# Kernel tuning notes

Measured on AMD Instinct MI355X. Metric: run time of the kernel, lower is better.

## Reference

```python
import jax, jax.numpy as jnp
import numpy as np

N0, N1, N2 = 400000, 75000, 15000
E1, E2 = 1200000, 240000
F_IN, NC = 64, 40
H1, C1 = 2, 8          # layer 1: heads=2, out_channels=8 -> concat dim 16
H2, C2 = 1, NC         # layer 2: heads=1, out_channels=num_classes
NEG_SLOPE = 0.2


def gat_conv(x_src, x_dst, src, dst, Ws, Wd, att_s, att_d, bias, heads, ch):
    """PyG GATConv on bipartite (x_src, x_dst) with remove+add self loops."""
    n_dst = x_dst.shape[0]
    hs = (x_src @ Ws).reshape(-1, heads, ch)   # [N_src, H, C]
    hd = (x_dst @ Wd).reshape(-1, heads, ch)   # [N_dst, H, C]
    a_s = (hs * att_s).sum(-1)                 # [N_src, H]
    a_d = (hd * att_d).sum(-1)                 # [N_dst, H]
    loops = jnp.arange(n_dst)
    src_all = jnp.concatenate([src, loops])
    dst_all = jnp.concatenate([dst, loops])
    # remove_self_loops: drop pre-existing i->i edges; add_self_loops: appended
    valid = jnp.concatenate([src != dst, jnp.ones(n_dst, dtype=bool)])[:, None]
    logits = jax.nn.leaky_relu(a_s[src_all] + a_d[dst_all], NEG_SLOPE)  # [E, H]
    logits = jnp.where(valid, logits, -jnp.inf)
    m = jax.ops.segment_max(logits, dst_all, num_segments=n_dst)        # [N_dst, H]
    w = jnp.where(valid, jnp.exp(logits - m[dst_all]), 0.0)
    denom = jax.ops.segment_sum(w, dst_all, num_segments=n_dst)
    alpha = w / denom[dst_all]                                          # [E, H]
    out = jax.ops.segment_sum(alpha[:, :, None] * hs[src_all], dst_all,
                              num_segments=n_dst)                       # [N_dst, H, C]
    return out.reshape(n_dst, heads * ch) + bias


def setup_inputs() -> dict:
    key = jax.random.key(0)
    ks = jax.random.split(key, 16)
    s = 0.1
    return {
        "x": jax.random.normal(ks[0], (N0, F_IN), dtype=jnp.float32),
        "e1_src": jax.random.randint(ks[1], (E1,), 0, N0),
        "e1_dst": jax.random.randint(ks[2], (E1,), 0, N1),
        "e2_src": jax.random.randint(ks[3], (E2,), 0, N1),
        "e2_dst": jax.random.randint(ks[4], (E2,), 0, N2),
        "W1s": jax.random.normal(ks[5], (F_IN, H1 * C1), dtype=jnp.float32) * s,
        "W1d": jax.random.normal(ks[6], (F_IN, H1 * C1), dtype=jnp.float32) * s,
        "att1_s": jax.random.normal(ks[7], (H1, C1), dtype=jnp.float32) * s,
        "att1_d": jax.random.normal(ks[8], (H1, C1), dtype=jnp.float32) * s,
        "b1": jnp.zeros((H1 * C1,), dtype=jnp.float32),
        "W2s": jax.random.normal(ks[9], (H1 * C1, H2 * C2), dtype=jnp.float32) * s,
        "W2d": jax.random.normal(ks[10], (H1 * C1, H2 * C2), dtype=jnp.float32) * s,
        "att2_s": jax.random.normal(ks[11], (H2, C2), dtype=jnp.float32) * s,
        "att2_d": jax.random.normal(ks[12], (H2, C2), dtype=jnp.float32) * s,
        "b2": jnp.zeros((H2 * C2,), dtype=jnp.float32),
    }


def reference(x, e1_src, e1_dst, e2_src, e2_dst,
              W1s, W1d, att1_s, att1_d, b1,
              W2s, W2d, att2_s, att2_d, b2):
    h = gat_conv(x, x[:N1], e1_src, e1_dst, W1s, W1d, att1_s, att1_d, b1, H1, C1)
    h = jax.nn.elu(h)
    o = gat_conv(h, h[:N2], e2_src, e2_dst, W2s, W2d, att2_s, att2_d, b2, H2, C2)
    return jax.nn.log_softmax(o, axis=-1)
```

## Files before the change

### kernel.cpp

```cpp
#include <hip/hip_runtime.h>
#include <hip/hip_bf16.h>

constexpr int N0 = 400000, N1 = 75000, N2 = 15000;
constexpr int E1 = 1200000, E2 = 240000;
constexpr int NC = 40;
constexpr float NEG_SLOPE = 0.2f;

constexpr int BK1 = 128;
constexpr int NB1 = (N1 + BK1 - 1) / BK1;
constexpr int CAPB1 = 2432;
constexpr int BK2 = 32;
constexpr int NB2 = (N2 + BK2 - 1) / BK2;
constexpr int CAPB2 = 704;

constexpr int TILE = 8192;
constexpr int NT1 = (E1 + TILE - 1) / TILE;
constexpr int NT2 = (E2 + TILE - 1) / TILE;
constexpr int BPJ = (N0 + 511) / 512;

using f32x4 = __attribute__((ext_vector_type(4))) float;
using s16x8 = __attribute__((ext_vector_type(8))) short;

__device__ __forceinline__ float leaky(float v) { return v > 0.f ? v : NEG_SLOPE * v; }

__device__ __forceinline__ unsigned cvtpk(float lo, float hi) {
    unsigned r;
    asm("v_cvt_pk_bf16_f32 %0, %1, %2" : "=v"(r) : "v"(lo), "v"(hi));
    return r;
}

__device__ __forceinline__ unsigned bf16pair(float lo, float hi) {
    unsigned a = __float_as_uint(lo), b = __float_as_uint(hi);
    a = (a + 0x7FFFu + ((a >> 16) & 1u)) >> 16;
    b = (b + 0x7FFFu + ((b >> 16) & 1u)) & 0xFFFF0000u;
    return a | b;
}
__device__ __forceinline__ float bfLo(unsigned w) { return __uint_as_float(w << 16); }
__device__ __forceinline__ float bfHi(unsigned w) { return __uint_as_float(w & 0xFFFF0000u); }

__global__ __launch_bounds__(256) void k1a_kernel(
    const int* __restrict__ e1s, const int* __restrict__ e1d,
    const int* __restrict__ e2s, const int* __restrict__ e2d,
    int* __restrict__ gcnt1, unsigned* __restrict__ bin1,
    int* __restrict__ gcnt2, unsigned* __restrict__ bin2)
{
    __shared__ int hist[NB1];
    __shared__ int gbase[NB1];

    const int bid = blockIdx.x;
    const int tid = threadIdx.x;
    const bool isL1 = bid < NT1;
    const int* es = isL1 ? e1s : e2s;
    const int* ed = isL1 ? e1d : e2d;
    const int nE = isL1 ? E1 : E2;
    const int nb = isL1 ? NB1 : NB2;
    const int cap = isL1 ? CAPB1 : CAPB2;
    const int shift = isL1 ? 7 : 5;
    const int lsh = isL1 ? 19 : 17;
    int* gc = isL1 ? gcnt1 : gcnt2;
    unsigned* gbin = isL1 ? bin1 : bin2;
    const int base = (isL1 ? bid : bid - NT1) * TILE;
    const int lim = min(TILE, nE - base);

    for (int b = tid; b < nb; b += 256) hist[b] = 0;
    __syncthreads();
    for (int i = tid; i < lim; i += 256) {
        int s = es[base + i], d = ed[base + i];
        if (s != d) atomicAdd(&hist[d >> shift], 1);
    }
    __syncthreads();
    for (int b = tid; b < nb; b += 256) {
        int c = hist[b];
        gbase[b] = (c > 0) ? atomicAdd(&gc[b], c) : 0;
        hist[b] = 0;
    }
    __syncthreads();
    for (int i = tid; i < lim; i += 256) {
        int s = es[base + i], d = ed[base + i];
        if (s != d) {
            int b = d >> shift;
            int pos = gbase[b] + atomicAdd(&hist[b], 1);
            if (pos < cap)
                gbin[(size_t)b * cap + pos] =
                    (unsigned)s | ((unsigned)(d & ((1 << shift) - 1)) << lsh);
        }
    }
}

__global__ __launch_bounds__(256, 2) void k1b_kernel(
    const float* __restrict__ x,
    const float* __restrict__ W1s, const float* __restrict__ W1d,
    const float* __restrict__ att1s, const float* __restrict__ att1d,
    unsigned* __restrict__ rec1, float* __restrict__ a_d1)
{
    __shared__ float2 vds[64];
    const int tid = threadIdx.x;
    const int l = tid & 63, nd = l & 15, kg = l >> 4, wv = tid >> 6;
    const int nodeBase = blockIdx.x * 512;
    const bool hasN1 = nodeBase < N1;

    if (hasN1) {
        if (tid < 64) {
            float d0 = 0.f, d1 = 0.f;
            const float* wr = W1d + (size_t)tid * 16;
            #pragma unroll
            for (int cc = 0; cc < 8; ++cc) {
                d0 = fmaf(wr[cc], att1d[cc], d0);
                d1 = fmaf(wr[8 + cc], att1d[8 + cc], d1);
            }
            vds[tid] = make_float2(d0, d1);
        }
        __syncthreads();
    }

    s16x8 bf0, bf1;
    {
        union { unsigned u[4]; s16x8 v; } t0, t1;
        #pragma unroll
        for (int q = 0; q < 4; ++q) {
            t0.u[q] = cvtpk(W1s[(8 * kg + 2 * q) * 16 + nd],
                            W1s[(8 * kg + 2 * q + 1) * 16 + nd]);
            t1.u[q] = cvtpk(W1s[(32 + 8 * kg + 2 * q) * 16 + nd],
                            W1s[(32 + 8 * kg + 2 * q + 1) * 16 + nd]);
        }
        bf0 = t0.v; bf1 = t1.v;
    }
    float att4[4];
    #pragma unroll
    for (int r = 0; r < 4; ++r) att4[r] = att1s[4 * kg + r];

    const int myBase = nodeBase + wv * 16 + nd;

    float4 P[4][4];

    auto LOADr = [&](int r, float4 (&Q)[4]) {
        int n = min(myBase + r * 64, N0 - 1);
        const float* xr_ = x + (size_t)n * 64 + 8 * kg;
        Q[0] = *(const float4*)(xr_);
        Q[1] = *(const float4*)(xr_ + 4);
        Q[2] = *(const float4*)(xr_ + 32);
        Q[3] = *(const float4*)(xr_ + 36);
    };

    #pragma unroll
    for (int r = 0; r < 4; ++r) LOADr(r, P[r]);

    #pragma unroll
    for (int r = 0; r < 8; ++r) {
        const int node = myBase + r * 64;
        float4 (&Q)[4] = P[r & 3];

        union { unsigned u[4]; s16x8 v; } a0, a1;
        a0.u[0] = cvtpk(Q[0].x, Q[0].y); a0.u[1] = cvtpk(Q[0].z, Q[0].w);
        a0.u[2] = cvtpk(Q[1].x, Q[1].y); a0.u[3] = cvtpk(Q[1].z, Q[1].w);
        a1.u[0] = cvtpk(Q[2].x, Q[2].y); a1.u[1] = cvtpk(Q[2].z, Q[2].w);
        a1.u[2] = cvtpk(Q[3].x, Q[3].y); a1.u[3] = cvtpk(Q[3].z, Q[3].w);

        float pd0 = 0.f, pd1 = 0.f;
        if (hasN1) {
            float xv8[16] = {Q[0].x, Q[0].y, Q[0].z, Q[0].w, Q[1].x, Q[1].y, Q[1].z, Q[1].w,
                             Q[2].x, Q[2].y, Q[2].z, Q[2].w, Q[3].x, Q[3].y, Q[3].z, Q[3].w};
            #pragma unroll
            for (int j = 0; j < 8; ++j) {
                float2 v = vds[8 * kg + j];
                pd0 = fmaf(xv8[j], v.x, pd0);
                pd1 = fmaf(xv8[j], v.y, pd1);
            }
            #pragma unroll
            for (int j = 0; j < 8; ++j) {
                float2 v = vds[32 + 8 * kg + j];
                pd0 = fmaf(xv8[8 + j], v.x, pd0);
                pd1 = fmaf(xv8[8 + j], v.y, pd1);
            }
        }

        if (r + 4 < 8) LOADr(r + 4, Q);
        __builtin_amdgcn_sched_barrier(0);

        f32x4 acc = {0.f, 0.f, 0.f, 0.f};
        acc = __builtin_amdgcn_mfma_f32_16x16x32_bf16(bf0, a0.v, acc, 0, 0, 0);
        acc = __builtin_amdgcn_mfma_f32_16x16x32_bf16(bf1, a1.v, acc, 0, 0, 0);

        float p = acc[0] * att4[0];
        p = fmaf(acc[1], att4[1], p);
        p = fmaf(acc[2], att4[2], p);
        p = fmaf(acc[3], att4[3], p);
        p += __shfl_xor(p, 16, 64);
        float q = __shfl_xor(p, 32, 64);

        if (node < N0) {
            unsigned* rp = rec1 + (size_t)node * 16;
            uint2 hw;
            hw.x = cvtpk(acc[0], acc[1]);
            hw.y = cvtpk(acc[2], acc[3]);
            *(uint2*)(rp + 2 * kg) = hw;
            if (kg == 0)
                *(uint4*)(rp + 8) = make_uint4(__float_as_uint(p), __float_as_uint(q), 0u, 0u);
            else if (kg == 1)
                *(uint4*)(rp + 12) = make_uint4(0u, 0u, 0u, 0u);
        }
        if (hasN1 && node < N1) {
            pd0 += __shfl_xor(pd0, 16, 64); pd0 += __shfl_xor(pd0, 32, 64);
            pd1 += __shfl_xor(pd1, 16, 64); pd1 += __shfl_xor(pd1, 32, 64);
            if (kg == 0)
                ((float2*)a_d1)[node] = make_float2(pd0, pd1);
        }
    }
}

__global__ __launch_bounds__(512) void k2_kernel(
    const int* __restrict__ gcnt1, const unsigned* __restrict__ bin1,
    const unsigned* __restrict__ rec1, const float* __restrict__ a_d1,
    const float* __restrict__ b1,
    const float* __restrict__ W2s, const float* __restrict__ W2d,
    const float* __restrict__ att2s, const float* __restrict__ att2d,
    unsigned* __restrict__ rec2)
{
    __shared__ unsigned srt[CAPB1];
    __shared__ int hist[BK1], start[BK1 + 1];
    __shared__ float w2sl[640], va[16], vd[16];
    __shared__ float h1s[BK1][17];

    const int b = blockIdx.x, tid = threadIdx.x;
    const int d0 = b * BK1;
    const int nN = min(BK1, N1 - d0);
    const int ncnt = min(gcnt1[b], CAPB1);
    const unsigned* bp = bin1 + (size_t)b * CAPB1;

    for (int i = tid; i < 640; i += 512) w2sl[i] = W2s[i];
    if (tid < BK1) hist[tid] = 0;
    if (tid >= 128 && tid < 144) {
        int k = tid - 128;
        float sa = 0.f, sd = 0.f;
        for (int cc = 0; cc < 40; ++cc) {
            sa = fmaf(W2s[k * 40 + cc], att2s[cc], sa);
            sd = fmaf(W2d[k * 40 + cc], att2d[cc], sd);
        }
        va[k] = sa; vd[k] = sd;
    }
    __syncthreads();
    for (int i = tid; i < ncnt; i += 512) atomicAdd(&hist[bp[i] >> 19], 1);
    __syncthreads();
    if (tid == 0) {
        int a = 0;
        for (int k = 0; k < BK1; ++k) { start[k] = a; a += hist[k]; }
        start[BK1] = a;
    }
    __syncthreads();
    if (tid < BK1) hist[tid] = start[tid];
    __syncthreads();
    for (int i = tid; i < ncnt; i += 512) {
        unsigned p = bp[i];
        int pos = atomicAdd(&hist[p >> 19], 1);
        srt[pos] = p & 0x7FFFFu;
    }
    __syncthreads();

    const int g = tid >> 4, c = tid & 15, h = c >> 3;
    const int wbase = tid & 48;
    const int wmap = (c < 8) ? c : (8 + ((c >> 2) & 1));
    for (int n = g; n < nN; n += 32) {
        const int node = d0 + n;
        const float ad = a_d1[(size_t)node * 2 + h];
        const int st = start[n], cnt = start[n + 1] - start[n];
        unsigned rw0 = rec1[(size_t)node * 16 + wmap];
        unsigned rw1 = (cnt >= 1) ? rec1[(size_t)srt[st] * 16 + wmap] : 0u;
        unsigned rw2 = (cnt >= 2) ? rec1[(size_t)srt[st + 1] * 16 + wmap] : 0u;
        unsigned rw3 = (cnt >= 3) ? rec1[(size_t)srt[st + 2] * 16 + wmap] : 0u;
        float accv = 0.f, den = 0.f;
        for (int j = 0; j <= cnt; ++j) {
            float asv = __uint_as_float((unsigned)__shfl((int)rw0, wbase + 8 + 4 * h, 64));
            unsigned chw = (unsigned)__shfl((int)rw0, wbase + (c >> 1), 64);
            float hv = (c & 1) ? bfHi(chw) : bfLo(chw);
            float w = __expf(leaky(asv + ad));
            accv = fmaf(w, hv, accv);
            den += w;
            rw0 = rw1; rw1 = rw2; rw2 = rw3;
            rw3 = (j + 4 <= cnt) ? rec1[(size_t)srt[st + j + 3] * 16 + wmap] : 0u;
        }
        float v = accv / den + b1[c];
        h1s[n][c] = v > 0.f ? v : (__expf(v) - 1.f);
    }
    __syncthreads();
    for (int i = tid; i < nN * 24; i += 512) {
        int nn = i / 24, w = i - nn * 24;
        unsigned* rp = rec2 + (size_t)(d0 + nn) * 24;
        if (w < 20) {
            int c0 = 2 * w, c1 = c0 + 1;
            float s0 = 0.f, s1 = 0.f;
            #pragma unroll
            for (int k = 0; k < 16; ++k) {
                float hk = h1s[nn][k];
                s0 = fmaf(hk, w2sl[k * 40 + c0], s0);
                s1 = fmaf(hk, w2sl[k * 40 + c1], s1);
            }
            rp[w] = bf16pair(s0, s1);
        } else if (w < 22) {
            const float* vv = (w == 20) ? va : vd;
            float s = 0.f;
            #pragma unroll
            for (int k = 0; k < 16; ++k) s = fmaf(h1s[nn][k], vv[k], s);
            rp[w] = __float_as_uint(s);
        }
    }
}

__global__ __launch_bounds__(1024) void k3_kernel(
    const int* __restrict__ gcnt2, const unsigned* __restrict__ bin2,
    const unsigned* __restrict__ rec2, const float* __restrict__ b2,
    float* __restrict__ out)
{
    __shared__ unsigned srt[CAPB2];
    __shared__ int hist[BK2], start[BK2 + 1];

    const int b = blockIdx.x, tid = threadIdx.x;
    const int d0 = b * BK2;
    const int nN = min(BK2, N2 - d0);
    const int ncnt = min(gcnt2[b], CAPB2);
    const unsigned* bp = bin2 + (size_t)b * CAPB2;

    if (tid < BK2) hist[tid] = 0;
    __syncthreads();
    for (int i = tid; i < ncnt; i += 1024) atomicAdd(&hist[bp[i] >> 17], 1);
    __syncthreads();
    if (tid == 0) {
        int a = 0;
        for (int k = 0; k < BK2; ++k) { start[k] = a; a += hist[k]; }
        start[BK2] = a;
    }
    __syncthreads();
    if (tid < BK2) hist[tid] = start[tid];
    __syncthreads();
    for (int i = tid; i < ncnt; i += 1024) {
        unsigned p = bp[i];
        int pos = atomicAdd(&hist[p >> 17], 1);
        srt[pos] = p & 0x1FFFFu;
    }
    __syncthreads();

    const int g = tid >> 5, l = tid & 31;
    const float bb0 = (l < 20) ? b2[2 * l] : 0.f;
    const float bb1 = (l < 20) ? b2[2 * l + 1] : 0.f;
    for (int n = g; n < nN; n += 32) {
        const int node = d0 + n;
        const int st = start[n], cnt = start[n + 1] - start[n];
        unsigned rw0 = (l < 22) ? rec2[(size_t)node * 24 + l] : 0u;
        const float ad = __uint_as_float((unsigned)__shfl((int)rw0, 21, 32));
        unsigned rw1 = (cnt >= 1 && l < 21) ? rec2[(size_t)srt[st] * 24 + l] : 0u;
        unsigned rw2 = (cnt >= 2 && l < 21) ? rec2[(size_t)srt[st + 1] * 24 + l] : 0u;
        unsigned rw3 = (cnt >= 3 && l < 21) ? rec2[(size_t)srt[st + 2] * 24 + l] : 0u;
        float a0 = 0.f, a1 = 0.f, den = 0.f;
        for (int j = 0; j <= cnt; ++j) {
            float asv = __uint_as_float((unsigned)__shfl((int)rw0, 20, 32));
            float w = __expf(leaky(asv + ad));
            a0 = fmaf(w, bfLo(rw0), a0);
            a1 = fmaf(w, bfHi(rw0), a1);
            den += w;
            rw0 = rw1; rw1 = rw2; rw2 = rw3;
            rw3 = (j + 4 <= cnt && l < 21) ? rec2[(size_t)srt[st + j + 3] * 24 + l] : 0u;
        }
        float v0 = (l < 20) ? a0 / den + bb0 : -3.4e38f;
        float v1 = (l < 20) ? a1 / den + bb1 : -3.4e38f;
        float mx = fmaxf(v0, v1);
        #pragma unroll
        for (int k = 16; k >= 1; k >>= 1) mx = fmaxf(mx, __shfl_xor(mx, k, 32));
        float ex = (l < 20) ? __expf(v0 - mx) + __expf(v1 - mx) : 0.f;
        #pragma unroll
        for (int k = 16; k >= 1; k >>= 1) ex += __shfl_xor(ex, k, 32);
        float lse = mx + logf(ex);
        if (l < 20)
            ((float2*)(out + (size_t)node * 40))[l] = make_float2(v0 - lse, v1 - lse);
    }
}

extern "C" void kernel_launch(void* const* d_in, const int* in_sizes, int n_in,
                              void* d_out, int out_size, void* d_ws, size_t ws_size,
                              hipStream_t stream) {
    const float* x      = (const float*)d_in[0];
    const int*   e1_src = (const int*)d_in[1];
    const int*   e1_dst = (const int*)d_in[2];
    const int*   e2_src = (const int*)d_in[3];
    const int*   e2_dst = (const int*)d_in[4];
    const float* W1s    = (const float*)d_in[5];
    const float* W1d    = (const float*)d_in[6];
    const float* att1s  = (const float*)d_in[7];
    const float* att1d  = (const float*)d_in[8];
    const float* b1     = (const float*)d_in[9];
    const float* W2s    = (const float*)d_in[10];
    const float* W2d    = (const float*)d_in[11];
    const float* att2s  = (const float*)d_in[12];
    const float* att2d  = (const float*)d_in[13];
    const float* b2     = (const float*)d_in[14];
    float* out = (float*)d_out;

    float* wsbase = (float*)d_ws;
    size_t o = 0;
    int*      gcnt1 = (int*)(wsbase + o);      o += NB1;
    int*      gcnt2 = (int*)(wsbase + o);      o += NB2;
    const size_t zeroWords = o;
    unsigned* bin1  = (unsigned*)(wsbase + o); o += (size_t)NB1 * CAPB1;
    unsigned* bin2  = (unsigned*)(wsbase + o); o += (size_t)NB2 * CAPB2;
    unsigned* rec1  = (unsigned*)(wsbase + o); o += (size_t)N0 * 16;
    float*    a_d1  = (float*)(wsbase + o);    o += (size_t)N1 * 2;
    unsigned* rec2  = (unsigned*)(wsbase + o); o += (size_t)N1 * 24;

    hipMemsetAsync(d_ws, 0, zeroWords * sizeof(float), stream);

    k1a_kernel<<<NT1 + NT2, 256, 0, stream>>>(
        e1_src, e1_dst, e2_src, e2_dst, gcnt1, bin1, gcnt2, bin2);

    k1b_kernel<<<BPJ, 256, 0, stream>>>(
        x, W1s, W1d, att1s, att1d, rec1, a_d1);

    k2_kernel<<<NB1, 512, 0, stream>>>(gcnt1, bin1, rec1, a_d1, b1,
                                       W2s, W2d, att2s, att2d, rec2);

    k3_kernel<<<NB2, 1024, 0, stream>>>(gcnt2, bin2, rec2, b2, out);
}
```

Measured before the change: 133.9 us.

## Fuse edge binning and layer-1 projection into one kernel launch with one node tile per block

Merges the edge-binning kernel and the x@W1s projection kernel into a single launch: the first blocks do the edge histogram and scatter, and the remaining blocks each project 64 nodes, one node per thread group, with no unrolled prefetch loop. This removes a kernel launch boundary and lets the two independent phases overlap on the GPU. In exchange, each projection block does far less work, so setup costs such as the W1d/att reduction and W1s bf16 packing are repeated across many more blocks. The software-pipelined x loads are also gone, so latency hiding now depends on occupancy. The fused kernel also carries the large shared histogram arrays, which may limit occupancy for the projection blocks.

```diff
diff --git a/kernel.cpp b/kernel.cpp
--- a/kernel.cpp
+++ b/kernel.cpp
@@ -16,7 +16,8 @@
 constexpr int TILE = 8192;
 constexpr int NT1 = (E1 + TILE - 1) / TILE;
 constexpr int NT2 = (E2 + TILE - 1) / TILE;
-constexpr int BPJ = (N0 + 511) / 512;
+constexpr int NTB = NT1 + NT2;
+constexpr int BPJ = N0 / 64;
 
 using f32x4 = __attribute__((ext_vector_type(4))) float;
 using s16x8 = __attribute__((ext_vector_type(8))) short;
@@ -38,65 +39,67 @@
 __device__ __forceinline__ float bfLo(unsigned w) { return __uint_as_float(w << 16); }
 __device__ __forceinline__ float bfHi(unsigned w) { return __uint_as_float(w & 0xFFFF0000u); }
 
-__global__ __launch_bounds__(256) void k1a_kernel(
+__global__ __launch_bounds__(256) void k1_kernel(
+    const float* __restrict__ x,
+    const float* __restrict__ W1s, const float* __restrict__ W1d,
+    const float* __restrict__ att1s, const float* __restrict__ att1d,
     const int* __restrict__ e1s, const int* __restrict__ e1d,
     const int* __restrict__ e2s, const int* __restrict__ e2d,
+    unsigned* __restrict__ rec1, float* __restrict__ a_d1,
     int* __restrict__ gcnt1, unsigned* __restrict__ bin1,
     int* __restrict__ gcnt2, unsigned* __restrict__ bin2)
 {
     __shared__ int hist[NB1];
     __shared__ int gbase[NB1];
-
-    const int bid = blockIdx.x;
+    __shared__ float2 vds[64];
+
+    int bid = blockIdx.x;
     const int tid = threadIdx.x;
-    const bool isL1 = bid < NT1;
-    const int* es = isL1 ? e1s : e2s;
-    const int* ed = isL1 ? e1d : e2d;
-    const int nE = isL1 ? E1 : E2;
-    const int nb = isL1 ? NB1 : NB2;
-    const int cap = isL1 ? CAPB1 : CAPB2;
-    const int shift = isL1 ? 7 : 5;
-    const int lsh = isL1 ? 19 : 17;
-    int* gc = isL1 ? gcnt1 : gcnt2;
-    unsigned* gbin = isL1 ? bin1 : bin2;
-    const int base = (isL1 ? bid : bid - NT1) * TILE;
-    const int lim = min(TILE, nE - base);
-
-    for (int b = tid; b < nb; b += 256) hist[b] = 0;
-    __syncthreads();
-    for (int i = tid; i < lim; i += 256) {
-        int s = es[base + i], d = ed[base + i];
-        if (s != d) atomicAdd(&hist[d >> shift], 1);
-    }
-    __syncthreads();
-    for (int b = tid; b < nb; b += 256) {
-        int c = hist[b];
-        gbase[b] = (c > 0) ? atomicAdd(&gc[b], c) : 0;
-        hist[b] = 0;
-    }
-    __syncthreads();
-    for (int i = tid; i < lim; i += 256) {
-        int s = es[base + i], d = ed[base + i];
-        if (s != d) {
-            int b = d >> shift;
-            int pos = gbase[b] + atomicAdd(&hist[b], 1);
-            if (pos < cap)
-                gbin[(size_t)b * cap + pos] =
-                    (unsigned)s | ((unsigned)(d & ((1 << shift) - 1)) << lsh);
-        }
-    }
-}
-
-__global__ __launch_bounds__(256, 2) void k1b_kernel(
-    const float* __restrict__ x,
-    const float* __restrict__ W1s, const float* __restrict__ W1d,
-    const float* __restrict__ att1s, const float* __restrict__ att1d,
-    unsigned* __restrict__ rec1, float* __restrict__ a_d1)
-{
-    __shared__ float2 vds[64];
-    const int tid = threadIdx.x;
-    const int l = tid & 63, nd = l & 15, kg = l >> 4, wv = tid >> 6;
-    const int nodeBase = blockIdx.x * 512;
+    if (bid < NTB) {
+        const bool isL1 = bid < NT1;
+        const int* es = isL1 ? e1s : e2s;
+        const int* ed = isL1 ? e1d : e2d;
+        const int nE = isL1 ? E1 : E2;
+        const int nb = isL1 ? NB1 : NB2;
+        const int cap = isL1 ? CAPB1 : CAPB2;
+        const int shift = isL1 ? 7 : 5;
+        const int lsh = isL1 ? 19 : 17;
+        int* gc = isL1 ? gcnt1 : gcnt2;
+        unsigned* gbin = isL1 ? bin1 : bin2;
+        const int base = (isL1 ? bid : bid - NT1) * TILE;
+        const int lim = min(TILE, nE - base);
+
+        for (int b = tid; b < nb; b += 256) hist[b] = 0;
+        __syncthreads();
+        for (int i = tid; i < lim; i += 256) {
+            int s = es[base + i], d = ed[base + i];
+            if (s != d) atomicAdd(&hist[d >> shift], 1);
+        }
+        __syncthreads();
+        for (int b = tid; b < nb; b += 256) {
+            int c = hist[b];
+            gbase[b] = (c > 0) ? atomicAdd(&gc[b], c) : 0;
+            hist[b] = 0;
+        }
+        __syncthreads();
+        for (int i = tid; i < lim; i += 256) {
+            int s = es[base + i], d = ed[base + i];
+            if (s != d) {
+                int b = d >> shift;
+                int pos = gbase[b] + atomicAdd(&hist[b], 1);
+                if (pos < cap)
+                    gbin[(size_t)b * cap + pos] =
+                        (unsigned)s | ((unsigned)(d & ((1 << shift) - 1)) << lsh);
+            }
+        }
+        return;
+    }
+    bid -= NTB;
+    const int l  = tid & 63;
+    const int nd = l & 15;
+    const int kg = l >> 4;
+    const int wv = tid >> 6;
+    const int nodeBase = bid * 64;
     const bool hasN1 = nodeBase < N1;
 
     if (hasN1) {
@@ -113,6 +116,14 @@
         __syncthreads();
     }
 
+    const int node = nodeBase + wv * 16 + nd;
+
+    const float* xr_ = x + (size_t)node * 64 + 8 * kg;
+    float4 q0 = *(const float4*)(xr_);
+    float4 q1 = *(const float4*)(xr_ + 4);
+    float4 q2 = *(const float4*)(xr_ + 32);
+    float4 q3 = *(const float4*)(xr_ + 36);
+
     s16x8 bf0, bf1;
     {
         union { unsigned u[4]; s16x8 v; } t0, t1;
@@ -129,82 +140,53 @@
     #pragma unroll
     for (int r = 0; r < 4; ++r) att4[r] = att1s[4 * kg + r];
 
-    const int myBase = nodeBase + wv * 16 + nd;
-
-    float4 P[4][4];
-
-    auto LOADr = [&](int r, float4 (&Q)[4]) {
-        int n = min(myBase + r * 64, N0 - 1);
-        const float* xr_ = x + (size_t)n * 64 + 8 * kg;
-        Q[0] = *(const float4*)(xr_);
-        Q[1] = *(const float4*)(xr_ + 4);
-        Q[2] = *(const float4*)(xr_ + 32);
-        Q[3] = *(const float4*)(xr_ + 36);
-    };
-
-    #pragma unroll
-    for (int r = 0; r < 4; ++r) LOADr(r, P[r]);
-
-    #pragma unroll
-    for (int r = 0; r < 8; ++r) {
-        const int node = myBase + r * 64;
-        float4 (&Q)[4] = P[r & 3];
-
-        union { unsigned u[4]; s16x8 v; } a0, a1;
-        a0.u[0] = cvtpk(Q[0].x, Q[0].y); a0.u[1] = cvtpk(Q[0].z, Q[0].w);
-        a0.u[2] = cvtpk(Q[1].x, Q[1].y); a0.u[3] = cvtpk(Q[1].z, Q[1].w);
-        a1.u[0] = cvtpk(Q[2].x, Q[2].y); a1.u[1] = cvtpk(Q[2].z, Q[2].w);
-        a1.u[2] = cvtpk(Q[3].x, Q[3].y); a1.u[3] = cvtpk(Q[3].z, Q[3].w);
-
+    union { unsigned u[4]; s16x8 v; } a0, a1;
+    a0.u[0] = cvtpk(q0.x, q0.y); a0.u[1] = cvtpk(q0.z, q0.w);
+    a0.u[2] = cvtpk(q1.x, q1.y); a0.u[3] = cvtpk(q1.z, q1.w);
+    a1.u[0] = cvtpk(q2.x, q2.y); a1.u[1] = cvtpk(q2.z, q2.w);
+    a1.u[2] = cvtpk(q3.x, q3.y); a1.u[3] = cvtpk(q3.z, q3.w);
+
+    f32x4 acc = {0.f, 0.f, 0.f, 0.f};
+    acc = __builtin_amdgcn_mfma_f32_16x16x32_bf16(bf0, a0.v, acc, 0, 0, 0);
+    acc = __builtin_amdgcn_mfma_f32_16x16x32_bf16(bf1, a1.v, acc, 0, 0, 0);
+
+    float p = acc[0] * att4[0];
+    p = fmaf(acc[1], att4[1], p);
+    p = fmaf(acc[2], att4[2], p);
+    p = fmaf(acc[3], att4[3], p);
+    p += __shfl_xor(p, 16, 64);
+    float q = __shfl_xor(p, 32, 64);
+
+    unsigned* rp = rec1 + (size_t)node * 16;
+    uint2 hw;
+    hw.x = cvtpk(acc[0], acc[1]);
+    hw.y = cvtpk(acc[2], acc[3]);
+    *(uint2*)(rp + 2 * kg) = hw;
+    if (kg == 0)
+        *(uint4*)(rp + 8) = make_uint4(__float_as_uint(p), __float_as_uint(q), 0u, 0u);
+    else if (kg == 1)
+        *(uint4*)(rp + 12) = make_uint4(0u, 0u, 0u, 0u);
+
+    if (hasN1 && node < N1) {
+        float xv8[16] = {q0.x, q0.y, q0.z, q0.w, q1.x, q1.y, q1.z, q1.w,
+                         q2.x, q2.y, q2.z, q2.w, q3.x, q3.y, q3.z, q3.w};
         float pd0 = 0.f, pd1 = 0.f;
-        if (hasN1) {
-            float xv8[16] = {Q[0].x, Q[0].y, Q[0].z, Q[0].w, Q[1].x, Q[1].y, Q[1].z, Q[1].w,
-                             Q[2].x, Q[2].y, Q[2].z, Q[2].w, Q[3].x, Q[3].y, Q[3].z, Q[3].w};
-            #pragma unroll
-            for (int j = 0; j < 8; ++j) {
-                float2 v = vds[8 * kg + j];
-                pd0 = fmaf(xv8[j], v.x, pd0);
-                pd1 = fmaf(xv8[j], v.y, pd1);
-            }
-            #pragma unroll
-            for (int j = 0; j < 8; ++j) {
-                float2 v = vds[32 + 8 * kg + j];
-                pd0 = fmaf(xv8[8 + j], v.x, pd0);
-                pd1 = fmaf(xv8[8 + j], v.y, pd1);
-            }
-        }
-
-        if (r + 4 < 8) LOADr(r + 4, Q);
-        __builtin_amdgcn_sched_barrier(0);
-
-        f32x4 acc = {0.f, 0.f, 0.f, 0.f};
-        acc = __builtin_amdgcn_mfma_f32_16x16x32_bf16(bf0, a0.v, acc, 0, 0, 0);
-        acc = __builtin_amdgcn_mfma_f32_16x16x32_bf16(bf1, a1.v, acc, 0, 0, 0);
-
-        float p = acc[0] * att4[0];
-        p = fmaf(acc[1], att4[1], p);
-        p = fmaf(acc[2], att4[2], p);
-        p = fmaf(acc[3], att4[3], p);
-        p += __shfl_xor(p, 16, 64);
-        float q = __shfl_xor(p, 32, 64);
-
-        if (node < N0) {
-            unsigned* rp = rec1 + (size_t)node * 16;
-            uint2 hw;
-            hw.x = cvtpk(acc[0], acc[1]);
-            hw.y = cvtpk(acc[2], acc[3]);
-            *(uint2*)(rp + 2 * kg) = hw;
-            if (kg == 0)
-                *(uint4*)(rp + 8) = make_uint4(__float_as_uint(p), __float_as_uint(q), 0u, 0u);
-            else if (kg == 1)
-                *(uint4*)(rp + 12) = make_uint4(0u, 0u, 0u, 0u);
-        }
-        if (hasN1 && node < N1) {
-            pd0 += __shfl_xor(pd0, 16, 64); pd0 += __shfl_xor(pd0, 32, 64);
-            pd1 += __shfl_xor(pd1, 16, 64); pd1 += __shfl_xor(pd1, 32, 64);
-            if (kg == 0)
-                ((float2*)a_d1)[node] = make_float2(pd0, pd1);
-        }
+        #pragma unroll
+        for (int j = 0; j < 8; ++j) {
+            float2 v = vds[8 * kg + j];
+            pd0 = fmaf(xv8[j], v.x, pd0);
+            pd1 = fmaf(xv8[j], v.y, pd1);
+        }
+        #pragma unroll
+        for (int j = 0; j < 8; ++j) {
+            float2 v = vds[32 + 8 * kg + j];
+            pd0 = fmaf(xv8[8 + j], v.x, pd0);
+            pd1 = fmaf(xv8[8 + j], v.y, pd1);
+        }
+        pd0 += __shfl_xor(pd0, 16, 64); pd0 += __shfl_xor(pd0, 32, 64);
+        pd1 += __shfl_xor(pd1, 16, 64); pd1 += __shfl_xor(pd1, 32, 64);
+        if (kg == 0)
+            ((float2*)a_d1)[node] = make_float2(pd0, pd1);
     }
 }
 
@@ -406,11 +388,9 @@
 
     hipMemsetAsync(d_ws, 0, zeroWords * sizeof(float), stream);
 
-    k1a_kernel<<<NT1 + NT2, 256, 0, stream>>>(
-        e1_src, e1_dst, e2_src, e2_dst, gcnt1, bin1, gcnt2, bin2);
-
-    k1b_kernel<<<BPJ, 256, 0, stream>>>(
-        x, W1s, W1d, att1s, att1d, rec1, a_d1);
+    k1_kernel<<<NTB + BPJ, 256, 0, stream>>>(
+        x, W1s, W1d, att1s, att1d, e1_src, e1_dst, e2_src, e2_dst,
+        rec1, a_d1, gcnt1, bin1, gcnt2, bin2);
 
     k2_kernel<<<NB1, 512, 0, stream>>>(gcnt1, bin1, rec1, a_d1, b1,
                                        W2s, W2d, att2s, att2d, rec2);
```

Measured after the change: 119.9 us. -10.5%, faster.
